# Kernel tuning notes

Measured on AMD Instinct MI355X. Metric: run time of the kernel, lower is better.

The kernel has to match this reference:

```python
import jax, jax.numpy as jnp
import numpy as np

def setup_inputs() -> dict:
    key = jax.random.key(0)
    x = jax.random.normal(key, (2, 16, 2048, 64), dtype=jnp.float32)
    return {"x": x}

def reference(x):
    # Unnormalized attention: scores = q k^T (no softmax, no scaling), out = scores v,
    # with q = k = v = x. Faithful to the two torch.einsum calls.
    scores = jnp.einsum('bhid,bhjd->bhij', x, x)   # [B,H,T,T]
    out = jnp.einsum('bhij,bhjd->bhid', scores, x)  # [B,H,T,D]
    return out
```

## Files before the change

kernel.cpp:

```cpp
#include <hip/hip_runtime.h>


#define TDIM 2048
#define DDIM 64
#define NHEADS 32
#define NCH 16

typedef float f4 __attribute__((ext_vector_type(4)));
typedef float f32x4 __attribute__((ext_vector_type(4)));
typedef short bf16x8 __attribute__((ext_vector_type(8)));
typedef short s4 __attribute__((ext_vector_type(4)));

__device__ __forceinline__ void async_copy16(const void* g, void* l) {
    __builtin_amdgcn_global_load_lds(
        (const __attribute__((address_space(1))) void*)g,
        (__attribute__((address_space(3))) void*)l, 16, 0, 0);
}

__device__ __forceinline__ short f2bf(float f) {
    unsigned u = __builtin_bit_cast(unsigned, f);
    unsigned r = (u + 0x7fffu + ((u >> 16) & 1u)) >> 16;
    return (short)r;
}
__device__ __forceinline__ float bf2f(short s) {
    return __builtin_bit_cast(float, ((unsigned)(unsigned short)s) << 16);
}

__device__ __forceinline__ const bf16x8* fragp(const short* base, int row,
                                               int rowlen, int kelem) {
    const char* p = (const char*)(base + row * rowlen);
    return (const bf16x8*)(p + ((kelem * 2) ^ ((row & 7) << 4)));
}

__global__ __launch_bounds__(256) void k1_gram(const float* __restrict__ x,
                                               short* __restrict__ part) {
    __shared__ __align__(16) short XT[64 * 128];

    const int b    = blockIdx.x;
    const int tid  = threadIdx.x;
    const int lane = tid & 63;
    const int w    = tid >> 6;
    const int head = b >> 4, ch = b & 15;

    const float* xh = x + ((size_t)head * TDIM + ch * 128) * DDIM;

    const int rg = tid >> 4, cg = tid & 15;
    const int r0 = rg * 8, c4 = cg * 4;

    f4 v[8];
#pragma unroll
    for (int k = 0; k < 8; ++k)
        v[k] = *reinterpret_cast<const f4*>(xh + (size_t)(r0 + k) * DDIM + c4);

#pragma unroll
    for (int j = 0; j < 4; ++j) {
        bf16x8 pk;
#pragma unroll
        for (int k = 0; k < 8; ++k) pk[k] = f2bf(v[k][j]);
        const int c = c4 + j;
        *(bf16x8*)((char*)XT + c * 256 + ((2 * r0) ^ ((c & 7) << 4))) = pk;
    }
    __syncthreads();

    const int li = lane & 15, g = lane >> 4;
    const int iq0 = (w >> 1) * 2, jq0 = (w & 1) * 2;

    f32x4 acc[2][2];
#pragma unroll
    for (int a = 0; a < 2; ++a)
#pragma unroll
        for (int q = 0; q < 2; ++q) acc[a][q] = (f32x4){0.f, 0.f, 0.f, 0.f};

#pragma unroll
    for (int k0 = 0; k0 < 128; k0 += 32) {
        bf16x8 af[2], bv[2];
        af[0] = *fragp(XT, (iq0 + 0) * 16 + li, 128, k0 + 8 * g);
        af[1] = *fragp(XT, (iq0 + 1) * 16 + li, 128, k0 + 8 * g);
        bv[0] = *fragp(XT, (jq0 + 0) * 16 + li, 128, k0 + 8 * g);
        bv[1] = *fragp(XT, (jq0 + 1) * 16 + li, 128, k0 + 8 * g);
#pragma unroll
        for (int a = 0; a < 2; ++a)
#pragma unroll
            for (int q = 0; q < 2; ++q)
                acc[a][q] = __builtin_amdgcn_mfma_f32_16x16x32_bf16(
                    af[a], bv[q], acc[a][q], 0, 0, 0);
    }

    short* pp = part + (size_t)b * 4096;
#pragma unroll
    for (int a = 0; a < 2; ++a)
#pragma unroll
        for (int d = 0; d < 2; ++d) {
            s4 pk;
#pragma unroll
            for (int q = 0; q < 4; ++q) pk[q] = f2bf(acc[a][d][q]);
            *(s4*)(pp + ((((w * 2 + a) * 2 + d) * 64 + lane) << 2)) = pk;
        }
}

__global__ __launch_bounds__(256) void k2a_reduce(const short* __restrict__ part,
                                                  short* __restrict__ gbf) {
    const int b    = blockIdx.x;
    const int tid  = threadIdx.x;
    const int head = b >> 2, quarter = b & 3;

    const int f = quarter * 256 + tid;
    const short* ph = part + (size_t)head * NCH * 4096 + (f << 2);

    float s[4] = {0.f, 0.f, 0.f, 0.f};
#pragma unroll
    for (int c = 0; c < NCH; ++c) {
        const s4 v = *reinterpret_cast<const s4*>(ph + (size_t)c * 4096);
#pragma unroll
        for (int q = 0; q < 4; ++q) s[q] += bf2f(v[q]);
    }

    const int lane = f & 63, wad = f >> 6;
    const int w = wad >> 2, a = (wad >> 1) & 1, d = wad & 1;
    const int g = lane >> 4, li = lane & 15;
    const int iq0 = (w >> 1) * 2, jq0 = (w & 1) * 2;
    const int j = (jq0 + d) * 16 + li;
    char* gb = (char*)gbf + (size_t)head * 8192;
#pragma unroll
    for (int q = 0; q < 4; ++q) {
        const int i = (iq0 + a) * 16 + g * 4 + q;
        *(short*)(gb + i * 128 + ((2 * j) ^ ((i & 7) << 4))) = f2bf(s[q]);
    }
}

__global__ __launch_bounds__(512) void k2b_xg(const float* __restrict__ x,
                                              float* __restrict__ out,
                                              const short* __restrict__ gbf) {
    __shared__ __align__(16) short Xb[8192];
    __shared__ __align__(16) short Gb[4096];

    const int b    = blockIdx.x;
    const int tid  = threadIdx.x;
    const int lane = tid & 63;
    const int w    = tid >> 6;
    const int head = b >> 4, ch = b & 15;

    {
        const short* gg = gbf + (size_t)head * 4096 + w * 512 + lane * 8;
        async_copy16(gg, Gb + w * 512);
    }

    const float* xh = x + ((size_t)head * TDIM + ch * 128) * DDIM;
#pragma unroll
    for (int e = 0; e < 4; ++e) {
        const int i4 = e * 512 + tid;
        const int r  = i4 >> 4;
        const int c4 = (i4 & 15) << 2;
        const f4 v = *reinterpret_cast<const f4*>(xh + (size_t)i4 * 4);
        s4 pk;
        pk[0] = f2bf(v[0]); pk[1] = f2bf(v[1]);
        pk[2] = f2bf(v[2]); pk[3] = f2bf(v[3]);
        *(s4*)((char*)Xb + r * 128 + ((2 * c4) ^ ((r & 7) << 4))) = pk;
    }
    __syncthreads();

    const int li = lane & 15, g = lane >> 4;

    f32x4 acc[4];
#pragma unroll
    for (int d = 0; d < 4; ++d) acc[d] = (f32x4){0.f, 0.f, 0.f, 0.f};

#pragma unroll
    for (int k0 = 0; k0 < 64; k0 += 32) {
        bf16x8 af, bv[4];
        af = *fragp(Xb, w * 16 + li, 64, k0 + 8 * g);
#pragma unroll
        for (int d = 0; d < 4; ++d)
            bv[d] = *fragp(Gb, d * 16 + li, 64, k0 + 8 * g);
#pragma unroll
        for (int d = 0; d < 4; ++d)
            acc[d] = __builtin_amdgcn_mfma_f32_16x16x32_bf16(
                af, bv[d], acc[d], 0, 0, 0);
    }

    float* oh = out + ((size_t)head * TDIM + ch * 128) * DDIM;
#pragma unroll
    for (int d = 0; d < 4; ++d)
#pragma unroll
        for (int q = 0; q < 4; ++q)
            oh[(w * 16 + g * 4 + q) * 64 + d * 16 + li] = acc[d][q];
}

extern "C" void kernel_launch(void* const* d_in, const int* in_sizes, int n_in,
                              void* d_out, int out_size, void* d_ws, size_t ws_size,
                              hipStream_t stream) {
    const float* x = (const float*)d_in[0];
    float* out  = (float*)d_out;
    short* part = (short*)d_ws;
    short* gbf  = part + (size_t)512 * 4096;

    k1_gram<<<NHEADS * NCH, 256, 0, stream>>>(x, part);
    k2a_reduce<<<128, 256, 0, stream>>>(part, gbf);
    k2b_xg<<<512, 512, 0, stream>>>(x, out, gbf);
}
```

Before: 18.69 us.

## Fuse partial Gram reduction into k1 via last-block atomic counter

Removes the separate k2a_reduce launch. Each k1 block stores its partial Gram tile with cache-bypassing stores and then increments a per-head atomic counter. The last-arriving block for each head sums the 16 partials and writes the swizzled bf16 Gram matrix. This saves a kernel launch and its gap, but adds a hipMemsetAsync to reset the counters and serializes each head's reduction onto a single block.

```diff
diff --git a/kernel.cpp b/kernel.cpp
--- a/kernel.cpp
+++ b/kernel.cpp
@@ -10,6 +10,7 @@
 typedef float f32x4 __attribute__((ext_vector_type(4)));
 typedef short bf16x8 __attribute__((ext_vector_type(8)));
 typedef short s4 __attribute__((ext_vector_type(4)));
+typedef int i2 __attribute__((ext_vector_type(2)));
 
 __device__ __forceinline__ void async_copy16(const void* g, void* l) {
     __builtin_amdgcn_global_load_lds(
@@ -26,6 +27,33 @@
     return __builtin_bit_cast(float, ((unsigned)(unsigned short)s) << 16);
 }
 
+__device__ __forceinline__ void st8_cc(void* p, i2 v) {
+    asm volatile("global_store_dwordx2 %0, %1, off sc0 sc1"
+                 :: "v"(p), "v"(v) : "memory");
+}
+__device__ __forceinline__ void ld8x2_cc(const short* p0, const short* p1,
+                                         const short* p2, const short* p3,
+                                         const short* p4, const short* p5,
+                                         const short* p6, const short* p7,
+                                         i2& v0, i2& v1, i2& v2, i2& v3,
+                                         i2& v4, i2& v5, i2& v6, i2& v7) {
+    asm volatile(
+        "global_load_dwordx2 %0, %8, off sc0 sc1\n\t"
+        "global_load_dwordx2 %1, %9, off sc0 sc1\n\t"
+        "global_load_dwordx2 %2, %10, off sc0 sc1\n\t"
+        "global_load_dwordx2 %3, %11, off sc0 sc1\n\t"
+        "global_load_dwordx2 %4, %12, off sc0 sc1\n\t"
+        "global_load_dwordx2 %5, %13, off sc0 sc1\n\t"
+        "global_load_dwordx2 %6, %14, off sc0 sc1\n\t"
+        "global_load_dwordx2 %7, %15, off sc0 sc1\n\t"
+        "s_waitcnt vmcnt(0)"
+        : "=&v"(v0), "=&v"(v1), "=&v"(v2), "=&v"(v3),
+          "=&v"(v4), "=&v"(v5), "=&v"(v6), "=&v"(v7)
+        : "v"(p0), "v"(p1), "v"(p2), "v"(p3),
+          "v"(p4), "v"(p5), "v"(p6), "v"(p7)
+        : "memory");
+}
+
 __device__ __forceinline__ const bf16x8* fragp(const short* base, int row,
                                                int rowlen, int kelem) {
     const char* p = (const char*)(base + row * rowlen);
@@ -33,8 +61,11 @@
 }
 
 __global__ __launch_bounds__(256) void k1_gram(const float* __restrict__ x,
-                                               short* __restrict__ part) {
+                                               short* __restrict__ part,
+                                               short* __restrict__ gbf,
+                                               unsigned* __restrict__ syncw) {
     __shared__ __align__(16) short XT[64 * 128];
+    __shared__ int is_last;
 
     const int b    = blockIdx.x;
     const int tid  = threadIdx.x;
@@ -94,37 +125,51 @@
             s4 pk;
 #pragma unroll
             for (int q = 0; q < 4; ++q) pk[q] = f2bf(acc[a][d][q]);
-            *(s4*)(pp + ((((w * 2 + a) * 2 + d) * 64 + lane) << 2)) = pk;
+            st8_cc(pp + ((((w * 2 + a) * 2 + d) * 64 + lane) << 2),
+                   __builtin_bit_cast(i2, pk));
         }
-}
-
-__global__ __launch_bounds__(256) void k2a_reduce(const short* __restrict__ part,
-                                                  short* __restrict__ gbf) {
-    const int b    = blockIdx.x;
-    const int tid  = threadIdx.x;
-    const int head = b >> 2, quarter = b & 3;
-
-    const int f = quarter * 256 + tid;
-    const short* ph = part + (size_t)head * NCH * 4096 + (f << 2);
-
-    float s[4] = {0.f, 0.f, 0.f, 0.f};
-#pragma unroll
-    for (int c = 0; c < NCH; ++c) {
-        const s4 v = *reinterpret_cast<const s4*>(ph + (size_t)c * 4096);
-#pragma unroll
-        for (int q = 0; q < 4; ++q) s[q] += bf2f(v[q]);
-    }
-
-    const int lane = f & 63, wad = f >> 6;
-    const int w = wad >> 2, a = (wad >> 1) & 1, d = wad & 1;
-    const int g = lane >> 4, li = lane & 15;
-    const int iq0 = (w >> 1) * 2, jq0 = (w & 1) * 2;
-    const int j = (jq0 + d) * 16 + li;
+    asm volatile("s_waitcnt vmcnt(0)" ::: "memory");
+    __syncthreads();
+
+    if (tid == 0) {
+        unsigned old = __hip_atomic_fetch_add(&syncw[head * 64], 1u,
+                                              __ATOMIC_RELAXED,
+                                              __HIP_MEMORY_SCOPE_AGENT);
+        is_last = (old == NCH - 1);
+    }
+    __syncthreads();
+    if (!is_last) return;
+
+    const short* ph = part + (size_t)head * NCH * 4096;
     char* gb = (char*)gbf + (size_t)head * 8192;
 #pragma unroll
-    for (int q = 0; q < 4; ++q) {
-        const int i = (iq0 + a) * 16 + g * 4 + q;
-        *(short*)(gb + i * 128 + ((2 * j) ^ ((i & 7) << 4))) = f2bf(s[q]);
+    for (int s = 0; s < 4; ++s) {
+        const int f = s * 256 + tid;
+        const short* p0 = ph + (f << 2);
+        i2 u[16];
+        ld8x2_cc(p0,              p0 + 4096,      p0 + 2 * 4096,  p0 + 3 * 4096,
+                 p0 + 4 * 4096,   p0 + 5 * 4096,  p0 + 6 * 4096,  p0 + 7 * 4096,
+                 u[0], u[1], u[2], u[3], u[4], u[5], u[6], u[7]);
+        ld8x2_cc(p0 + 8 * 4096,   p0 + 9 * 4096,  p0 + 10 * 4096, p0 + 11 * 4096,
+                 p0 + 12 * 4096,  p0 + 13 * 4096, p0 + 14 * 4096, p0 + 15 * 4096,
+                 u[8], u[9], u[10], u[11], u[12], u[13], u[14], u[15]);
+        float sm[4] = {0.f, 0.f, 0.f, 0.f};
+#pragma unroll
+        for (int c = 0; c < 16; ++c) {
+            const s4 pv = __builtin_bit_cast(s4, u[c]);
+#pragma unroll
+            for (int q = 0; q < 4; ++q) sm[q] += bf2f(pv[q]);
+        }
+        const int ln = f & 63, wad = f >> 6;
+        const int ww = wad >> 2, aa = (wad >> 1) & 1, dd = wad & 1;
+        const int gg = ln >> 4, ll = ln & 15;
+        const int j = ((ww & 1) * 2 + dd) * 16 + ll;
+        const int ib = ((ww >> 1) * 2 + aa) * 16 + gg * 4;
+#pragma unroll
+        for (int q = 0; q < 4; ++q) {
+            const int i = ib + q;
+            *(short*)(gb + i * 128 + ((2 * j) ^ ((i & 7) << 4))) = f2bf(sm[q]);
+        }
     }
 }
 
@@ -193,8 +238,9 @@
     float* out  = (float*)d_out;
     short* part = (short*)d_ws;
     short* gbf  = part + (size_t)512 * 4096;
-
-    k1_gram<<<NHEADS * NCH, 256, 0, stream>>>(x, part);
-    k2a_reduce<<<128, 256, 0, stream>>>(part, gbf);
+    unsigned* syncw = (unsigned*)(gbf + (size_t)NHEADS * 4096);
+
+    (void)hipMemsetAsync(syncw, 0, 8192, stream);
+    k1_gram<<<NHEADS * NCH, 256, 0, stream>>>(x, part, gbf, syncw);
     k2b_xg<<<512, 512, 0, stream>>>(x, out, gbf);
 }
```

Result: slower. 26.68 us (+42.8%).

## Fuse partial Gram reduction into the XG kernel, dropping a launch

Applied to the files above, without the earlier changes.

Removes the separate reduction kernel. Each XG block now sums the 16 per-chunk partial Gram matrices of its head itself and writes the bf16 result straight into swizzled shared memory. This saves one kernel launch and the global round trip of the reduced Gram. In exchange, the reduction is repeated 16 times per head across blocks, which adds extra L2 reads of the partials. The x loads are hoisted ahead of the reduction so their latency overlaps with it.

```diff
diff --git a/kernel.cpp b/kernel.cpp
--- a/kernel.cpp
+++ b/kernel.cpp
@@ -10,12 +10,6 @@
 typedef float f32x4 __attribute__((ext_vector_type(4)));
 typedef short bf16x8 __attribute__((ext_vector_type(8)));
 typedef short s4 __attribute__((ext_vector_type(4)));
-
-__device__ __forceinline__ void async_copy16(const void* g, void* l) {
-    __builtin_amdgcn_global_load_lds(
-        (const __attribute__((address_space(1))) void*)g,
-        (__attribute__((address_space(3))) void*)l, 16, 0, 0);
-}
 
 __device__ __forceinline__ short f2bf(float f) {
     unsigned u = __builtin_bit_cast(unsigned, f);
@@ -98,39 +92,9 @@
         }
 }
 
-__global__ __launch_bounds__(256) void k2a_reduce(const short* __restrict__ part,
-                                                  short* __restrict__ gbf) {
-    const int b    = blockIdx.x;
-    const int tid  = threadIdx.x;
-    const int head = b >> 2, quarter = b & 3;
-
-    const int f = quarter * 256 + tid;
-    const short* ph = part + (size_t)head * NCH * 4096 + (f << 2);
-
-    float s[4] = {0.f, 0.f, 0.f, 0.f};
-#pragma unroll
-    for (int c = 0; c < NCH; ++c) {
-        const s4 v = *reinterpret_cast<const s4*>(ph + (size_t)c * 4096);
-#pragma unroll
-        for (int q = 0; q < 4; ++q) s[q] += bf2f(v[q]);
-    }
-
-    const int lane = f & 63, wad = f >> 6;
-    const int w = wad >> 2, a = (wad >> 1) & 1, d = wad & 1;
-    const int g = lane >> 4, li = lane & 15;
-    const int iq0 = (w >> 1) * 2, jq0 = (w & 1) * 2;
-    const int j = (jq0 + d) * 16 + li;
-    char* gb = (char*)gbf + (size_t)head * 8192;
-#pragma unroll
-    for (int q = 0; q < 4; ++q) {
-        const int i = (iq0 + a) * 16 + g * 4 + q;
-        *(short*)(gb + i * 128 + ((2 * j) ^ ((i & 7) << 4))) = f2bf(s[q]);
-    }
-}
-
 __global__ __launch_bounds__(512) void k2b_xg(const float* __restrict__ x,
                                               float* __restrict__ out,
-                                              const short* __restrict__ gbf) {
+                                              const short* __restrict__ part) {
     __shared__ __align__(16) short Xb[8192];
     __shared__ __align__(16) short Gb[4096];
 
@@ -140,21 +104,45 @@
     const int w    = tid >> 6;
     const int head = b >> 4, ch = b & 15;
 
-    {
-        const short* gg = gbf + (size_t)head * 4096 + w * 512 + lane * 8;
-        async_copy16(gg, Gb + w * 512);
+    const float* xh = x + ((size_t)head * TDIM + ch * 128) * DDIM;
+    f4 v[4];
+#pragma unroll
+    for (int e = 0; e < 4; ++e)
+        v[e] = *reinterpret_cast<const f4*>(xh + (size_t)(e * 512 + tid) * 4);
+
+    const short* ph = part + (size_t)head * NCH * 4096;
+#pragma unroll
+    for (int sl = 0; sl < 2; ++sl) {
+        const int f = sl * 512 + tid;
+        const short* p0 = ph + (f << 2);
+        float s[4] = {0.f, 0.f, 0.f, 0.f};
+#pragma unroll
+        for (int c = 0; c < NCH; ++c) {
+            const s4 pv = *reinterpret_cast<const s4*>(p0 + (size_t)c * 4096);
+#pragma unroll
+            for (int q = 0; q < 4; ++q) s[q] += bf2f(pv[q]);
+        }
+        const int ln = f & 63, wad = f >> 6;
+        const int ww = wad >> 2, aa = (wad >> 1) & 1, dd = wad & 1;
+        const int gg = ln >> 4, ll = ln & 15;
+        const int j = ((ww & 1) * 2 + dd) * 16 + ll;
+        const int ib = ((ww >> 1) * 2 + aa) * 16 + gg * 4;
+#pragma unroll
+        for (int q = 0; q < 4; ++q) {
+            const int i = ib + q;
+            *(short*)((char*)Gb + i * 128 + ((2 * j) ^ ((i & 7) << 4))) =
+                f2bf(s[q]);
+        }
     }
 
-    const float* xh = x + ((size_t)head * TDIM + ch * 128) * DDIM;
 #pragma unroll
     for (int e = 0; e < 4; ++e) {
         const int i4 = e * 512 + tid;
         const int r  = i4 >> 4;
         const int c4 = (i4 & 15) << 2;
-        const f4 v = *reinterpret_cast<const f4*>(xh + (size_t)i4 * 4);
         s4 pk;
-        pk[0] = f2bf(v[0]); pk[1] = f2bf(v[1]);
-        pk[2] = f2bf(v[2]); pk[3] = f2bf(v[3]);
+        pk[0] = f2bf(v[e][0]); pk[1] = f2bf(v[e][1]);
+        pk[2] = f2bf(v[e][2]); pk[3] = f2bf(v[e][3]);
         *(s4*)((char*)Xb + r * 128 + ((2 * c4) ^ ((r & 7) << 4))) = pk;
     }
     __syncthreads();
@@ -192,9 +180,7 @@
     const float* x = (const float*)d_in[0];
     float* out  = (float*)d_out;
     short* part = (short*)d_ws;
-    short* gbf  = part + (size_t)512 * 4096;
 
     k1_gram<<<NHEADS * NCH, 256, 0, stream>>>(x, part);
-    k2a_reduce<<<128, 256, 0, stream>>>(part, gbf);
-    k2b_xg<<<512, 512, 0, stream>>>(x, out, gbf);
+    k2b_xg<<<512, 512, 0, stream>>>(x, out, part);
 }
```

Result: slower. 21.79 us (+16.6%).
